# Kernel optimization log

Measured on AMD Instinct MI355X. Metric: run time of the kernel, lower is better.

The kernel has to match this reference:

```python
import jax, jax.numpy as jnp
import numpy as np

B, T, D, N = 16, 1024, 1024, 8


def setup_inputs() -> dict:
    key = jax.random.key(0)
    k1, k2, k3, k4 = jax.random.split(key, 4)
    s = 1.0 / np.sqrt(D)
    return {
        "x": jax.random.normal(k1, (B, T, D), dtype=jnp.float32),
        "W_h": jax.random.normal(k2, (D, D), dtype=jnp.float32) * (0.9 * s),
        "W_x": jax.random.normal(k3, (D, D), dtype=jnp.float32) * s,
        "b_h": jnp.zeros((D,), dtype=jnp.float32),
        "W_write": jax.random.normal(k4, (D, D), dtype=jnp.float32) * s,
    }


def reference(x, W_h, W_x, b_h, W_write):
    Bs, Ts, Ds = x.shape
    scale = 1.0 / Ds ** 0.5
    x_proj = jnp.einsum('btd,ed->bte', x, W_x)  # x @ W_x.T
    h_tape0 = jnp.zeros((Bs, N, Ds), dtype=x.dtype)
    h_work0 = jnp.zeros((Bs, Ds), dtype=x.dtype)

    def step(carry, x_t):
        h_tape, h_work = carry
        read_scores = jnp.einsum('bd,bnd->bn', h_work, h_tape) * scale
        read_attn = jax.nn.softmax(read_scores, axis=-1)
        read_val = jnp.einsum('bn,bnd->bd', read_attn, h_tape)
        Rh = h_work @ W_h.T
        h_work_new = jnp.tanh(x_t + Rh + read_val + b_h)
        write_val = h_work_new @ W_write.T
        write_scores = jnp.einsum('bd,bnd->bn', write_val, h_tape) * scale
        write_attn = jax.nn.softmax(write_scores, axis=-1)
        wa = write_attn[..., None]  # [B,N,1]
        h_tape_new = h_tape * (1.0 - wa) + write_val[:, None, :] * wa
        return (h_tape_new, h_work_new), h_work_new

    (h_tape_final, _), h_work_all = jax.lax.scan(
        step, (h_tape0, h_work0), jnp.swapaxes(x_proj, 0, 1))
    h_work_all = jnp.swapaxes(h_work_all, 0, 1)  # [B,T,D]
    return h_work_all, h_tape_final, h_work_all[:, -1, :]
```

## Files before the change

kernel.cpp:

```cpp
#include <hip/hip_runtime.h>
#include <math.h>

typedef __bf16 bf16x8 __attribute__((ext_vector_type(8)));
typedef float f32x4 __attribute__((ext_vector_type(4)));

namespace {

constexpr int kB = 16;
constexpr int kT = 1024;
constexpr int kD = 1024;
constexpr int kN = 8;
constexpr float kScale = 0.03125f;

constexpr unsigned long long kSent = ~0ull;
constexpr unsigned kSentW = 0xFFFFFFFFu;
constexpr int kHS = 3 * kB * kD;
constexpr int kRW = 2 * kB * kD;

__device__ inline unsigned short f2bf(float f) {
  unsigned u = __float_as_uint(f);
  u += 0x7FFFu + ((u >> 16) & 1u);
  return (unsigned short)(u >> 16);
}
__device__ inline float bf2f(unsigned short b) {
  return __uint_as_float(((unsigned)b) << 16);
}

__device__ inline void atst8(void* p, unsigned long long v) {
  __hip_atomic_store((unsigned long long*)p, v, __ATOMIC_RELAXED,
                     __HIP_MEMORY_SCOPE_AGENT);
}
__device__ inline unsigned long long atld8(const void* p) {
  return __hip_atomic_load((unsigned long long*)p, __ATOMIC_RELAXED,
                           __HIP_MEMORY_SCOPE_AGENT);
}
__device__ inline void atstf(float* p, float v) {
  __hip_atomic_store(p, v, __ATOMIC_RELAXED, __HIP_MEMORY_SCOPE_AGENT);
}
__device__ inline void atstu(unsigned* p, unsigned v) {
  __hip_atomic_store(p, v, __ATOMIC_RELAXED, __HIP_MEMORY_SCOPE_AGENT);
}
__device__ inline unsigned atldu(const unsigned* p) {
  return __hip_atomic_load((unsigned*)p, __ATOMIC_RELAXED,
                           __HIP_MEMORY_SCOPE_AGENT);
}

union U16 { unsigned long long ll[2]; unsigned wrd[4]; bf16x8 bv; float4 f4; };

__global__ __launch_bounds__(256)
void xproj_kernel(const float* __restrict__ X, const float* __restrict__ Wx,
                  float* __restrict__ C) {
  __shared__ float Xs[16][132];
  __shared__ float Ws[16][132];
  const int tid = threadIdx.x;
  const int n0 = blockIdx.x * 128;
  const int m0 = blockIdx.y * 128;
  const int tx = tid & 15;
  const int ty = tid >> 4;
  const int lr = tid >> 2;
  const int lc = (tid & 3) * 4;

  float acc[8][8];
#pragma unroll
  for (int i = 0; i < 8; ++i)
#pragma unroll
    for (int j = 0; j < 8; ++j) acc[i][j] = 0.f;

  for (int k0 = 0; k0 < kD; k0 += 16) {
    const float4 xa = *(const float4*)&X[(size_t)(m0 + lr) * kD + k0 + lc];
    const float4 xb = *(const float4*)&X[(size_t)(m0 + lr + 64) * kD + k0 + lc];
    const float4 wa = *(const float4*)&Wx[(size_t)(n0 + lr) * kD + k0 + lc];
    const float4 wb = *(const float4*)&Wx[(size_t)(n0 + lr + 64) * kD + k0 + lc];
    __syncthreads();
    Xs[lc + 0][lr] = xa.x; Xs[lc + 1][lr] = xa.y; Xs[lc + 2][lr] = xa.z; Xs[lc + 3][lr] = xa.w;
    Xs[lc + 0][lr + 64] = xb.x; Xs[lc + 1][lr + 64] = xb.y; Xs[lc + 2][lr + 64] = xb.z; Xs[lc + 3][lr + 64] = xb.w;
    Ws[lc + 0][lr] = wa.x; Ws[lc + 1][lr] = wa.y; Ws[lc + 2][lr] = wa.z; Ws[lc + 3][lr] = wa.w;
    Ws[lc + 0][lr + 64] = wb.x; Ws[lc + 1][lr + 64] = wb.y; Ws[lc + 2][lr + 64] = wb.z; Ws[lc + 3][lr + 64] = wb.w;
    __syncthreads();
#pragma unroll
    for (int k = 0; k < 16; ++k) {
      float a[8], b[8];
      *(float4*)&a[0] = *(const float4*)&Xs[k][ty * 8];
      *(float4*)&a[4] = *(const float4*)&Xs[k][ty * 8 + 4];
      *(float4*)&b[0] = *(const float4*)&Ws[k][tx * 8];
      *(float4*)&b[4] = *(const float4*)&Ws[k][tx * 8 + 4];
#pragma unroll
      for (int i = 0; i < 8; ++i)
#pragma unroll
        for (int j = 0; j < 8; ++j) acc[i][j] += a[i] * b[j];
    }
  }
#pragma unroll
  for (int i = 0; i < 8; ++i) {
    float4 v0 = make_float4(acc[i][0], acc[i][1], acc[i][2], acc[i][3]);
    float4 v1 = make_float4(acc[i][4], acc[i][5], acc[i][6], acc[i][7]);
    float* p = &C[(size_t)(m0 + ty * 8 + i) * kD + n0 + tx * 8];
    *(float4*)p = v0;
    *(float4*)(p + 4) = v1;
  }
}

__device__ inline void store_split(unsigned short* hs, int b, int d4, float4 h) {
  union { unsigned short u[4]; unsigned long long ll; } c2, c1, c0;
  float hv[4] = {h.x, h.y, h.z, h.w};
#pragma unroll
  for (int e = 0; e < 4; ++e) {
    unsigned short x = f2bf(hv[e]);
    float r = hv[e] - bf2f(x);
    unsigned short y = f2bf(r);
    float r2 = r - bf2f(y);
    unsigned short z = f2bf(r2);
    c2.u[e] = x; c1.u[e] = y; c0.u[e] = z;
  }
  const int w = d4 >> 8;
  const int j = (d4 >> 5) & 7;
  const int q = (d4 >> 3) & 3;
  const int hf = (d4 >> 2) & 1;
  const int off = ((w * 8 + j) << 9) + (hf << 8) + ((q * 16 + b) << 2);
  atst8(&hs[0 * 16384 + off], c2.ll);
  atst8(&hs[1 * 16384 + off], c1.ll);
  atst8(&hs[2 * 16384 + off], c0.ll);
}

__global__ __launch_bounds__(256, 1)
void scan_kernel(const float* __restrict__ Wh, const float* __restrict__ Ww,
                 const float* __restrict__ bh,
                 float* __restrict__ hall,
                 unsigned short* __restrict__ hsplit,
                 float* __restrict__ rw,
                 unsigned* __restrict__ hmark,
                 float* __restrict__ out_tape,
                 float* __restrict__ out_h) {
  const int g = blockIdx.x;
  const int tid = threadIdx.x;
  const int w = tid >> 6;
  const int ln = tid & 63;
  const int bat = ln & 15;
  const int q = ln >> 4;
  const bool tapeb = (g < kB);
  const int col0 = (g & 31) * 32;
  const int matw = g >> 5;

  __shared__ float tp[kN][kD];
  __shared__ f32x4 Cred[2][4][2][64];
  __shared__ float red2[4][16];

  bf16x8 wf[3][2][8];
  {
    const float* Wsrc = matw ? Ww : Wh;
#pragma unroll
    for (int ct = 0; ct < 2; ++ct)
#pragma unroll
      for (int j = 0; j < 8; ++j) {
        const float* src = &Wsrc[(size_t)(col0 + ct * 16 + bat) * kD + (w * 8 + j) * 32 + q * 8];
        float v[8];
        *(float4*)&v[0] = *(const float4*)src;
        *(float4*)&v[4] = *(const float4*)(src + 4);
        union { unsigned short u[8]; bf16x8 b; } e2, e1, e0;
#pragma unroll
        for (int e = 0; e < 8; ++e) {
          unsigned short a = f2bf(v[e]);
          float r = v[e] - bf2f(a);
          unsigned short b2 = f2bf(r);
          float r2 = r - bf2f(b2);
          unsigned short c = f2bf(r2);
          e2.u[e] = a; e1.u[e] = b2; e0.u[e] = c;
        }
        wf[0][ct][j] = e2.b;
        wf[1][ct][j] = e1.b;
        wf[2][ct][j] = e0.b;
      }
  }

  float4 hprev = make_float4(0.f, 0.f, 0.f, 0.f);
  float4 bh4 = make_float4(0.f, 0.f, 0.f, 0.f);
  const int d4 = tid * 4;
  if (tapeb) {
    const size_t x0 = (size_t)g * kT * kD + d4;
    float4 xp0 = *(const float4*)&hall[x0];
    hprev.x = tanhf(xp0.x); hprev.y = tanhf(xp0.y);
    hprev.z = tanhf(xp0.z); hprev.w = tanhf(xp0.w);
    *(float4*)&hall[x0] = hprev;
    store_split(hsplit, g, d4, hprev);
    asm volatile("s_waitcnt vmcnt(0)" ::: "memory");
    if (ln == 0) atstu(&hmark[(w * 16 + g) * 16], 1u);
    bh4 = *(const float4*)&bh[d4];
    float4 z = make_float4(0.f, 0.f, 0.f, 0.f);
#pragma unroll
    for (int i = 0; i < 8; ++i) ((float4*)&tp[0][0])[i * 256 + tid] = z;
    __syncthreads();
  }

  for (int t = 0; t < kT; ++t) {
    const int p = t & 1;
    const unsigned short* hb = hsplit + p * kHS;

    float4 xp4 = make_float4(0.f, 0.f, 0.f, 0.f);
    if (tapeb && t < kT - 1)
      xp4 = *(const float4*)&hall[((size_t)g * kT + (t + 1)) * kD + d4];

    {
      const unsigned need = (unsigned)(t + 1);
      const unsigned* mk = &hmark[(w * 16 + bat) * 16];
      for (;;) {
        unsigned v = 0;
        if (q == 0) v = atldu(mk);
        v = __shfl(v, bat);
        if (v >= need) break;
        __builtin_amdgcn_s_sleep(1);
      }
      asm volatile("" ::: "memory");
    }
    bf16x8 af[3][8];
    const unsigned short* hw0 = hb + (w << 12) + (ln << 2);
#pragma unroll
    for (int j = 0; j < 8; ++j) {
      const unsigned short* p0 = hw0 + (j << 9);
#pragma unroll
      for (int part = 0; part < 3; ++part) {
        U16 u;
        u.ll[0] = atld8(p0 + part * 16384);
        u.ll[1] = atld8(p0 + part * 16384 + 256);
        af[part][j] = u.bv;
      }
    }

    f32x4 zf = {0.f, 0.f, 0.f, 0.f};
    f32x4 acc[2][2] = {{zf, zf}, {zf, zf}};
#pragma unroll
    for (int j = 0; j < 8; ++j) {
      const int s = j & 1;
#pragma unroll
      for (int ct = 0; ct < 2; ++ct) {
        f32x4 a = acc[ct][s];
        a = __builtin_amdgcn_mfma_f32_16x16x32_bf16(af[0][j], wf[0][ct][j], a, 0, 0, 0);
        a = __builtin_amdgcn_mfma_f32_16x16x32_bf16(af[0][j], wf[1][ct][j], a, 0, 0, 0);
        a = __builtin_amdgcn_mfma_f32_16x16x32_bf16(af[1][j], wf[0][ct][j], a, 0, 0, 0);
        a = __builtin_amdgcn_mfma_f32_16x16x32_bf16(af[0][j], wf[2][ct][j], a, 0, 0, 0);
        a = __builtin_amdgcn_mfma_f32_16x16x32_bf16(af[2][j], wf[0][ct][j], a, 0, 0, 0);
        a = __builtin_amdgcn_mfma_f32_16x16x32_bf16(af[1][j], wf[1][ct][j], a, 0, 0, 0);
        acc[ct][s] = a;
      }
    }
    Cred[p][w][0][ln] = acc[0][0] + acc[0][1];
    Cred[p][w][1][ln] = acc[1][0] + acc[1][1];
    __syncthreads();
    if (tid < 128) {
      const int ct = tid >> 6, l2 = tid & 63;
      f32x4 sv = Cred[p][0][ct][l2] + Cred[p][1][ct][l2] +
                 Cred[p][2][ct][l2] + Cred[p][3][ct][l2];
      float* dst = rw + p * kRW + matw * (kB * kD);
      const int col = col0 + ct * 16 + (l2 & 15);
      const int m0 = (l2 >> 4) * 4;
#pragma unroll
      for (int r = 0; r < 4; ++r) atstf(&dst[(size_t)(m0 + r) * kD + col], sv[r]);
    }

    if (!tapeb) continue;

    const int b = g;
    float* rwp = rw + p * kRW;
    float* pr = &rwp[b * kD + d4];
    float* pw = &rwp[kB * kD + b * kD + d4];
    float4 rh4, wv4;
    for (;;) {
      U16 ur, uw;
      ur.ll[0] = atld8(pr); ur.ll[1] = atld8(pr + 2);
      uw.ll[0] = atld8(pw); uw.ll[1] = atld8(pw + 2);
      int bad = 0;
#pragma unroll
      for (int k2 = 0; k2 < 4; ++k2)
        bad |= (ur.wrd[k2] == kSentW) | (uw.wrd[k2] == kSentW);
      if (!bad) { rh4 = ur.f4; wv4 = uw.f4; break; }
      __builtin_amdgcn_s_sleep(1);
    }
    asm volatile("" ::: "memory");
    atst8(pr, kSent); atst8(pr + 2, kSent);
    atst8(pw, kSent); atst8(pw + 2, kSent);

    float part[kN];
#pragma unroll
    for (int n = 0; n < kN; ++n) {
      const float4 tv = *(const float4*)&tp[n][d4];
      part[n] = wv4.x * tv.x + wv4.y * tv.y + wv4.z * tv.z + wv4.w * tv.w;
    }
#pragma unroll
    for (int off = 32; off > 0; off >>= 1)
#pragma unroll
      for (int n = 0; n < kN; ++n) part[n] += __shfl_xor(part[n], off);
    if (ln == 0)
#pragma unroll
      for (int n = 0; n < kN; ++n) red2[w][n] = part[n];
    __syncthreads();

    float wa[kN];
    {
      float mx = -1e30f;
#pragma unroll
      for (int n = 0; n < kN; ++n) {
        const float sc = kScale * (red2[0][n] + red2[1][n] + red2[2][n] + red2[3][n]);
        wa[n] = sc;
        mx = fmaxf(mx, sc);
      }
      float ssum = 0.f;
#pragma unroll
      for (int n = 0; n < kN; ++n) { wa[n] = expf(wa[n] - mx); ssum += wa[n]; }
      const float inv = 1.f / ssum;
#pragma unroll
      for (int n = 0; n < kN; ++n) wa[n] *= inv;
    }

#pragma unroll
    for (int n = 0; n < kN; ++n) {
      float4 tv = *(const float4*)&tp[n][d4];
      const float wn = wa[n], om = 1.f - wn;
      tv.x = tv.x * om + wv4.x * wn; tv.y = tv.y * om + wv4.y * wn;
      tv.z = tv.z * om + wv4.z * wn; tv.w = tv.w * om + wv4.w * wn;
      *(float4*)&tp[n][d4] = tv;
    }

    if (t == kT - 1) {
#pragma unroll
      for (int n = 0; n < kN; ++n) {
        const float4 tv = *(const float4*)&tp[n][d4];
        *(float4*)&out_tape[((size_t)b * kN + n) * kD + d4] = tv;
      }
      *(float4*)&out_h[b * kD + d4] = hprev;
      continue;
    }

#pragma unroll
    for (int n = 0; n < kN; ++n) {
      const float4 tv = *(const float4*)&tp[n][d4];
      part[n] = hprev.x * tv.x + hprev.y * tv.y + hprev.z * tv.z + hprev.w * tv.w;
    }
#pragma unroll
    for (int off = 32; off > 0; off >>= 1)
#pragma unroll
      for (int n = 0; n < kN; ++n) part[n] += __shfl_xor(part[n], off);
    if (ln == 0)
#pragma unroll
      for (int n = 0; n < kN; ++n) red2[w][8 + n] = part[n];
    __syncthreads();

    float ra[kN];
    {
      float mx = -1e30f;
#pragma unroll
      for (int n = 0; n < kN; ++n) {
        const float sc = kScale * (red2[0][8 + n] + red2[1][8 + n] + red2[2][8 + n] + red2[3][8 + n]);
        ra[n] = sc;
        mx = fmaxf(mx, sc);
      }
      float ssum = 0.f;
#pragma unroll
      for (int n = 0; n < kN; ++n) { ra[n] = expf(ra[n] - mx); ssum += ra[n]; }
      const float inv = 1.f / ssum;
#pragma unroll
      for (int n = 0; n < kN; ++n) ra[n] *= inv;
    }

    float4 rv = make_float4(0.f, 0.f, 0.f, 0.f);
#pragma unroll
    for (int n = 0; n < kN; ++n) {
      const float4 tv = *(const float4*)&tp[n][d4];
      rv.x += ra[n] * tv.x; rv.y += ra[n] * tv.y;
      rv.z += ra[n] * tv.z; rv.w += ra[n] * tv.w;
    }

    float4 hn;
    hn.x = tanhf(xp4.x + rh4.x + rv.x + bh4.x);
    hn.y = tanhf(xp4.y + rh4.y + rv.y + bh4.y);
    hn.z = tanhf(xp4.z + rh4.z + rv.z + bh4.z);
    hn.w = tanhf(xp4.w + rh4.w + rv.w + bh4.w);

    *(float4*)&hall[((size_t)b * kT + (t + 1)) * kD + d4] = hn;
    store_split(hsplit + (p ^ 1) * kHS, b, d4, hn);
    hprev = hn;

    asm volatile("s_waitcnt vmcnt(0)" ::: "memory");
    if (ln == 0) atstu(&hmark[(w * 16 + b) * 16], (unsigned)(t + 2));
  }
}

}

extern "C" void kernel_launch(void* const* d_in, const int* in_sizes, int n_in,
                              void* d_out, int out_size, void* d_ws, size_t ws_size,
                              hipStream_t stream) {
  const float* x  = (const float*)d_in[0];
  const float* Wh = (const float*)d_in[1];
  const float* Wx = (const float*)d_in[2];
  const float* bh = (const float*)d_in[3];
  const float* Ww = (const float*)d_in[4];

  float* out = (float*)d_out;
  float* hall = out;
  float* out_tape = out + (size_t)kB * kT * kD;
  float* out_h = out_tape + (size_t)kB * kN * kD;

  unsigned* hmark = (unsigned*)d_ws;
  unsigned short* hsplit = (unsigned short*)((char*)d_ws + 4096);
  float* rw = (float*)((char*)d_ws + 4096 + 2 * kHS * (int)sizeof(unsigned short));

  hipMemsetAsync(d_ws, 0, 4096, stream);
  hipMemsetAsync((void*)rw, 0xFF, 2 * kRW * sizeof(float), stream);

  xproj_kernel<<<dim3(kD / 128, (kB * kT) / 128), 256, 0, stream>>>(x, Wx, hall);

  scan_kernel<<<64, 256, 0, stream>>>(Wh, Ww, bh, hall, hsplit, rw, hmark,
                                      out_tape, out_h);
}
```

Baseline: 10.80 ms.

## Publish per-wave partial sums directly and fold read scores algebraically

Each wave now writes its own MFMA partial tile straight to global memory, so the cross-wave shared-memory reduction and its block barrier on the critical path go away. Consumers sum the four partials themselves. The read-attention scores are derived algebraically from pre-update tape dot products plus an h·write_val term, which merges the two reductions into one barrier. The Rh partials are polled later so the write path overlaps with them. The cost is four times more sentinel polling and global loads per consumer, and a small change in floating-point summation order.

```diff
diff --git a/kernel.cpp b/kernel.cpp
--- a/kernel.cpp
+++ b/kernel.cpp
@@ -15,7 +15,7 @@
 constexpr unsigned long long kSent = ~0ull;
 constexpr unsigned kSentW = 0xFFFFFFFFu;
 constexpr int kHS = 3 * kB * kD;
-constexpr int kRW = 2 * kB * kD;
+constexpr int kRWP = 2 * 32 * 4 * 512;
 
 __device__ inline unsigned short f2bf(float f) {
   unsigned u = __float_as_uint(f);
@@ -142,8 +142,7 @@
   const int matw = g >> 5;
 
   __shared__ float tp[kN][kD];
-  __shared__ f32x4 Cred[2][4][2][64];
-  __shared__ float red2[4][16];
+  __shared__ float red2[2][4][20];
 
   bf16x8 wf[3][2][8];
   {
@@ -171,6 +170,8 @@
         wf[2][ct][j] = e0.b;
       }
   }
+
+  float* const pbase0 = rw + ((size_t)((matw * 32 + (g & 31)) * 4 + w)) * 512;
 
   float4 hprev = make_float4(0.f, 0.f, 0.f, 0.f);
   float4 bh4 = make_float4(0.f, 0.f, 0.f, 0.f);
@@ -194,6 +195,7 @@
   for (int t = 0; t < kT; ++t) {
     const int p = t & 1;
     const unsigned short* hb = hsplit + p * kHS;
+    float* const rwP = rw + (size_t)p * kRWP;
 
     float4 xp4 = make_float4(0.f, 0.f, 0.f, 0.f);
     if (tapeb && t < kT - 1)
@@ -242,113 +244,151 @@
         acc[ct][s] = a;
       }
     }
-    Cred[p][w][0][ln] = acc[0][0] + acc[0][1];
-    Cred[p][w][1][ln] = acc[1][0] + acc[1][1];
+    {
+      const f32x4 a0 = acc[0][0] + acc[0][1];
+      const f32x4 a1 = acc[1][0] + acc[1][1];
+      float* base = pbase0 + (size_t)p * kRWP;
+      const int cc = ln & 15;
+      const int m0r = (ln >> 4) * 4;
+#pragma unroll
+      for (int r = 0; r < 4; ++r) {
+        atstf(&base[(m0r + r) * 32 + cc], a0[r]);
+        atstf(&base[(m0r + r) * 32 + 16 + cc], a1[r]);
+      }
+    }
+
+    if (!tapeb) continue;
+
+    const int b = g;
+    const int cb = d4 >> 5;
+    const int c0 = d4 & 31;
+    float* bwv = rwP + ((size_t)(32 + cb) * 4) * 512 + b * 32 + c0;
+    float* brh = rwP + ((size_t)cb * 4) * 512 + b * 32 + c0;
+
+    U16 vw[4];
+#pragma unroll
+    for (int k = 0; k < 4; ++k) {
+      vw[k].ll[0] = atld8(bwv + k * 512);
+      vw[k].ll[1] = atld8(bwv + k * 512 + 2);
+    }
+
+    {
+      float part[kN];
+#pragma unroll
+      for (int n = 0; n < kN; ++n) {
+        const float4 tv = *(const float4*)&tp[n][d4];
+        part[n] = hprev.x * tv.x + hprev.y * tv.y + hprev.z * tv.z + hprev.w * tv.w;
+      }
+#pragma unroll
+      for (int off = 32; off > 0; off >>= 1)
+#pragma unroll
+        for (int n = 0; n < kN; ++n) part[n] += __shfl_xor(part[n], off);
+      if (ln == 0)
+#pragma unroll
+        for (int n = 0; n < kN; ++n) red2[p][w][8 + n] = part[n];
+    }
+
+    for (;;) {
+      int bad = 0;
+#pragma unroll
+      for (int k = 0; k < 4; ++k)
+#pragma unroll
+        for (int k2 = 0; k2 < 4; ++k2) bad |= (vw[k].wrd[k2] == kSentW);
+      if (!bad) break;
+      __builtin_amdgcn_s_sleep(1);
+#pragma unroll
+      for (int k = 0; k < 4; ++k) {
+        vw[k].ll[0] = atld8(bwv + k * 512);
+        vw[k].ll[1] = atld8(bwv + k * 512 + 2);
+      }
+    }
+    asm volatile("" ::: "memory");
+#pragma unroll
+    for (int k = 0; k < 4; ++k) {
+      atst8(bwv + k * 512, kSent); atst8(bwv + k * 512 + 2, kSent);
+    }
+    float4 wv4;
+    wv4.x = ((vw[0].f4.x + vw[1].f4.x) + vw[2].f4.x) + vw[3].f4.x;
+    wv4.y = ((vw[0].f4.y + vw[1].f4.y) + vw[2].f4.y) + vw[3].f4.y;
+    wv4.z = ((vw[0].f4.z + vw[1].f4.z) + vw[2].f4.z) + vw[3].f4.z;
+    wv4.w = ((vw[0].f4.w + vw[1].f4.w) + vw[2].f4.w) + vw[3].f4.w;
+
+    U16 vr[4];
+#pragma unroll
+    for (int k = 0; k < 4; ++k) {
+      vr[k].ll[0] = atld8(brh + k * 512);
+      vr[k].ll[1] = atld8(brh + k * 512 + 2);
+    }
+
+    {
+      float part[9];
+#pragma unroll
+      for (int n = 0; n < kN; ++n) {
+        const float4 tv = *(const float4*)&tp[n][d4];
+        part[n] = wv4.x * tv.x + wv4.y * tv.y + wv4.z * tv.z + wv4.w * tv.w;
+      }
+      part[8] = hprev.x * wv4.x + hprev.y * wv4.y + hprev.z * wv4.z + hprev.w * wv4.w;
+#pragma unroll
+      for (int off = 32; off > 0; off >>= 1)
+#pragma unroll
+        for (int n = 0; n < 9; ++n) part[n] += __shfl_xor(part[n], off);
+      if (ln == 0) {
+#pragma unroll
+        for (int n = 0; n < kN; ++n) red2[p][w][n] = part[n];
+        red2[p][w][16] = part[8];
+      }
+    }
     __syncthreads();
-    if (tid < 128) {
-      const int ct = tid >> 6, l2 = tid & 63;
-      f32x4 sv = Cred[p][0][ct][l2] + Cred[p][1][ct][l2] +
-                 Cred[p][2][ct][l2] + Cred[p][3][ct][l2];
-      float* dst = rw + p * kRW + matw * (kB * kD);
-      const int col = col0 + ct * 16 + (l2 & 15);
-      const int m0 = (l2 >> 4) * 4;
-#pragma unroll
-      for (int r = 0; r < 4; ++r) atstf(&dst[(size_t)(m0 + r) * kD + col], sv[r]);
-    }
-
-    if (!tapeb) continue;
-
-    const int b = g;
-    float* rwp = rw + p * kRW;
-    float* pr = &rwp[b * kD + d4];
-    float* pw = &rwp[kB * kD + b * kD + d4];
-    float4 rh4, wv4;
-    for (;;) {
-      U16 ur, uw;
-      ur.ll[0] = atld8(pr); ur.ll[1] = atld8(pr + 2);
-      uw.ll[0] = atld8(pw); uw.ll[1] = atld8(pw + 2);
-      int bad = 0;
-#pragma unroll
-      for (int k2 = 0; k2 < 4; ++k2)
-        bad |= (ur.wrd[k2] == kSentW) | (uw.wrd[k2] == kSentW);
-      if (!bad) { rh4 = ur.f4; wv4 = uw.f4; break; }
-      __builtin_amdgcn_s_sleep(1);
-    }
-    asm volatile("" ::: "memory");
-    atst8(pr, kSent); atst8(pr + 2, kSent);
-    atst8(pw, kSent); atst8(pw + 2, kSent);
-
-    float part[kN];
+
+    float s_wv[kN], s_h[kN], s_hwv;
+#pragma unroll
+    for (int n = 0; n < kN; ++n) {
+      s_wv[n] = ((red2[p][0][n] + red2[p][1][n]) + red2[p][2][n]) + red2[p][3][n];
+      s_h[n] = ((red2[p][0][8 + n] + red2[p][1][8 + n]) + red2[p][2][8 + n]) + red2[p][3][8 + n];
+    }
+    s_hwv = ((red2[p][0][16] + red2[p][1][16]) + red2[p][2][16]) + red2[p][3][16];
+
+    float wa[kN];
+    {
+      float mx = -1e30f;
+#pragma unroll
+      for (int n = 0; n < kN; ++n) {
+        const float sc = kScale * s_wv[n];
+        wa[n] = sc;
+        mx = fmaxf(mx, sc);
+      }
+      float ssum = 0.f;
+#pragma unroll
+      for (int n = 0; n < kN; ++n) { wa[n] = expf(wa[n] - mx); ssum += wa[n]; }
+      const float inv = 1.f / ssum;
+#pragma unroll
+      for (int n = 0; n < kN; ++n) wa[n] *= inv;
+    }
+
+    float4 tpn[kN];
 #pragma unroll
     for (int n = 0; n < kN; ++n) {
       const float4 tv = *(const float4*)&tp[n][d4];
-      part[n] = wv4.x * tv.x + wv4.y * tv.y + wv4.z * tv.z + wv4.w * tv.w;
-    }
-#pragma unroll
-    for (int off = 32; off > 0; off >>= 1)
-#pragma unroll
-      for (int n = 0; n < kN; ++n) part[n] += __shfl_xor(part[n], off);
-    if (ln == 0)
-#pragma unroll
-      for (int n = 0; n < kN; ++n) red2[w][n] = part[n];
-    __syncthreads();
-
-    float wa[kN];
-    {
-      float mx = -1e30f;
-#pragma unroll
-      for (int n = 0; n < kN; ++n) {
-        const float sc = kScale * (red2[0][n] + red2[1][n] + red2[2][n] + red2[3][n]);
-        wa[n] = sc;
-        mx = fmaxf(mx, sc);
-      }
-      float ssum = 0.f;
-#pragma unroll
-      for (int n = 0; n < kN; ++n) { wa[n] = expf(wa[n] - mx); ssum += wa[n]; }
-      const float inv = 1.f / ssum;
-#pragma unroll
-      for (int n = 0; n < kN; ++n) wa[n] *= inv;
-    }
-
-#pragma unroll
-    for (int n = 0; n < kN; ++n) {
-      float4 tv = *(const float4*)&tp[n][d4];
       const float wn = wa[n], om = 1.f - wn;
-      tv.x = tv.x * om + wv4.x * wn; tv.y = tv.y * om + wv4.y * wn;
-      tv.z = tv.z * om + wv4.z * wn; tv.w = tv.w * om + wv4.w * wn;
-      *(float4*)&tp[n][d4] = tv;
+      tpn[n].x = tv.x * om + wv4.x * wn; tpn[n].y = tv.y * om + wv4.y * wn;
+      tpn[n].z = tv.z * om + wv4.z * wn; tpn[n].w = tv.w * om + wv4.w * wn;
+      *(float4*)&tp[n][d4] = tpn[n];
     }
 
     if (t == kT - 1) {
 #pragma unroll
-      for (int n = 0; n < kN; ++n) {
-        const float4 tv = *(const float4*)&tp[n][d4];
-        *(float4*)&out_tape[((size_t)b * kN + n) * kD + d4] = tv;
-      }
+      for (int n = 0; n < kN; ++n)
+        *(float4*)&out_tape[((size_t)b * kN + n) * kD + d4] = tpn[n];
       *(float4*)&out_h[b * kD + d4] = hprev;
       continue;
     }
 
-#pragma unroll
-    for (int n = 0; n < kN; ++n) {
-      const float4 tv = *(const float4*)&tp[n][d4];
-      part[n] = hprev.x * tv.x + hprev.y * tv.y + hprev.z * tv.z + hprev.w * tv.w;
-    }
-#pragma unroll
-    for (int off = 32; off > 0; off >>= 1)
-#pragma unroll
-      for (int n = 0; n < kN; ++n) part[n] += __shfl_xor(part[n], off);
-    if (ln == 0)
-#pragma unroll
-      for (int n = 0; n < kN; ++n) red2[w][8 + n] = part[n];
-    __syncthreads();
-
     float ra[kN];
     {
       float mx = -1e30f;
 #pragma unroll
       for (int n = 0; n < kN; ++n) {
-        const float sc = kScale * (red2[0][8 + n] + red2[1][8 + n] + red2[2][8 + n] + red2[3][8 + n]);
+        const float sc = kScale * (s_h[n] * (1.f - wa[n]) + s_hwv * wa[n]);
         ra[n] = sc;
         mx = fmaxf(mx, sc);
       }
@@ -363,10 +403,34 @@
     float4 rv = make_float4(0.f, 0.f, 0.f, 0.f);
 #pragma unroll
     for (int n = 0; n < kN; ++n) {
-      const float4 tv = *(const float4*)&tp[n][d4];
-      rv.x += ra[n] * tv.x; rv.y += ra[n] * tv.y;
-      rv.z += ra[n] * tv.z; rv.w += ra[n] * tv.w;
-    }
+      rv.x += ra[n] * tpn[n].x; rv.y += ra[n] * tpn[n].y;
+      rv.z += ra[n] * tpn[n].z; rv.w += ra[n] * tpn[n].w;
+    }
+
+    for (;;) {
+      int bad = 0;
+#pragma unroll
+      for (int k = 0; k < 4; ++k)
+#pragma unroll
+        for (int k2 = 0; k2 < 4; ++k2) bad |= (vr[k].wrd[k2] == kSentW);
+      if (!bad) break;
+      __builtin_amdgcn_s_sleep(1);
+#pragma unroll
+      for (int k = 0; k < 4; ++k) {
+        vr[k].ll[0] = atld8(brh + k * 512);
+        vr[k].ll[1] = atld8(brh + k * 512 + 2);
+      }
+    }
+    asm volatile("" ::: "memory");
+#pragma unroll
+    for (int k = 0; k < 4; ++k) {
+      atst8(brh + k * 512, kSent); atst8(brh + k * 512 + 2, kSent);
+    }
+    float4 rh4;
+    rh4.x = ((vr[0].f4.x + vr[1].f4.x) + vr[2].f4.x) + vr[3].f4.x;
+    rh4.y = ((vr[0].f4.y + vr[1].f4.y) + vr[2].f4.y) + vr[3].f4.y;
+    rh4.z = ((vr[0].f4.z + vr[1].f4.z) + vr[2].f4.z) + vr[3].f4.z;
+    rh4.w = ((vr[0].f4.w + vr[1].f4.w) + vr[2].f4.w) + vr[3].f4.w;
 
     float4 hn;
     hn.x = tanhf(xp4.x + rh4.x + rv.x + bh4.x);
@@ -404,7 +468,7 @@
   float* rw = (float*)((char*)d_ws + 4096 + 2 * kHS * (int)sizeof(unsigned short));
 
   hipMemsetAsync(d_ws, 0, 4096, stream);
-  hipMemsetAsync((void*)rw, 0xFF, 2 * kRW * sizeof(float), stream);
+  hipMemsetAsync((void*)rw, 0xFF, 2 * kRWP * sizeof(float), stream);
 
   xproj_kernel<<<dim3(kD / 128, (kB * kT) / 128), 256, 0, stream>>>(x, Wx, hall);
 
```

Measured after the change: 10.92 ms. No clear change (+1.2%).

## Use sentinel-poisoned hidden-state buffer to validate reads instead of strict flag ordering

Applied to the files above, without the earlier changes.

The split bf16 hidden-state buffer is now poisoned with a sentinel value, both at launch and after each consumer has read it. Readers spin until none of the loaded words equals the sentinel, so data validity is checked directly rather than relying only on the marker flag. The hall store is moved after the marker update, so the next step's consumers are signalled earlier. This adds extra sentinel stores and retry loads per step, and a valid bf16 pattern could in principle collide with the sentinel.

```diff
diff --git a/kernel.cpp b/kernel.cpp
--- a/kernel.cpp
+++ b/kernel.cpp
@@ -211,19 +211,28 @@
       }
       asm volatile("" ::: "memory");
     }
-    bf16x8 af[3][8];
+    U16 uf[3][8];
     const unsigned short* hw0 = hb + (w << 12) + (ln << 2);
-#pragma unroll
-    for (int j = 0; j < 8; ++j) {
-      const unsigned short* p0 = hw0 + (j << 9);
-#pragma unroll
-      for (int part = 0; part < 3; ++part) {
-        U16 u;
-        u.ll[0] = atld8(p0 + part * 16384);
-        u.ll[1] = atld8(p0 + part * 16384 + 256);
-        af[part][j] = u.bv;
-      }
-    }
+    for (;;) {
+      int bad = 0;
+#pragma unroll
+      for (int j = 0; j < 8; ++j) {
+        const unsigned short* p0 = hw0 + (j << 9);
+#pragma unroll
+        for (int part = 0; part < 3; ++part) {
+          uf[part][j].ll[0] = atld8(p0 + part * 16384);
+          uf[part][j].ll[1] = atld8(p0 + part * 16384 + 256);
+        }
+      }
+#pragma unroll
+      for (int j = 0; j < 8; ++j)
+#pragma unroll
+        for (int part = 0; part < 3; ++part)
+          bad |= (uf[part][j].ll[0] == kSent) | (uf[part][j].ll[1] == kSent);
+      if (!bad) break;
+      __builtin_amdgcn_s_sleep(1);
+    }
+    asm volatile("" ::: "memory");
 
     f32x4 zf = {0.f, 0.f, 0.f, 0.f};
     f32x4 acc[2][2] = {{zf, zf}, {zf, zf}};
@@ -233,12 +242,12 @@
 #pragma unroll
       for (int ct = 0; ct < 2; ++ct) {
         f32x4 a = acc[ct][s];
-        a = __builtin_amdgcn_mfma_f32_16x16x32_bf16(af[0][j], wf[0][ct][j], a, 0, 0, 0);
-        a = __builtin_amdgcn_mfma_f32_16x16x32_bf16(af[0][j], wf[1][ct][j], a, 0, 0, 0);
-        a = __builtin_amdgcn_mfma_f32_16x16x32_bf16(af[1][j], wf[0][ct][j], a, 0, 0, 0);
-        a = __builtin_amdgcn_mfma_f32_16x16x32_bf16(af[0][j], wf[2][ct][j], a, 0, 0, 0);
-        a = __builtin_amdgcn_mfma_f32_16x16x32_bf16(af[2][j], wf[0][ct][j], a, 0, 0, 0);
-        a = __builtin_amdgcn_mfma_f32_16x16x32_bf16(af[1][j], wf[1][ct][j], a, 0, 0, 0);
+        a = __builtin_amdgcn_mfma_f32_16x16x32_bf16(uf[0][j].bv, wf[0][ct][j], a, 0, 0, 0);
+        a = __builtin_amdgcn_mfma_f32_16x16x32_bf16(uf[0][j].bv, wf[1][ct][j], a, 0, 0, 0);
+        a = __builtin_amdgcn_mfma_f32_16x16x32_bf16(uf[1][j].bv, wf[0][ct][j], a, 0, 0, 0);
+        a = __builtin_amdgcn_mfma_f32_16x16x32_bf16(uf[0][j].bv, wf[2][ct][j], a, 0, 0, 0);
+        a = __builtin_amdgcn_mfma_f32_16x16x32_bf16(uf[2][j].bv, wf[0][ct][j], a, 0, 0, 0);
+        a = __builtin_amdgcn_mfma_f32_16x16x32_bf16(uf[1][j].bv, wf[1][ct][j], a, 0, 0, 0);
         acc[ct][s] = a;
       }
     }
@@ -293,6 +302,15 @@
       for (int n = 0; n < kN; ++n) red2[w][n] = part[n];
     __syncthreads();
 
+    {
+      unsigned short* hp0 = hsplit + p * kHS;
+      const int off = (((d4 >> 8) * 8 + ((d4 >> 5) & 7)) << 9) +
+                      (((d4 >> 2) & 1) << 8) + ((((d4 >> 3) & 3) * 16 + b) << 2);
+      atst8(&hp0[0 * 16384 + off], kSent);
+      atst8(&hp0[1 * 16384 + off], kSent);
+      atst8(&hp0[2 * 16384 + off], kSent);
+    }
+
     float wa[kN];
     {
       float mx = -1e30f;
@@ -374,12 +392,11 @@
     hn.z = tanhf(xp4.z + rh4.z + rv.z + bh4.z);
     hn.w = tanhf(xp4.w + rh4.w + rv.w + bh4.w);
 
+    asm volatile("s_waitcnt vmcnt(0)" ::: "memory");
+    store_split(hsplit + (p ^ 1) * kHS, b, d4, hn);
+    if (ln == 0) atstu(&hmark[(w * 16 + b) * 16], (unsigned)(t + 2));
     *(float4*)&hall[((size_t)b * kT + (t + 1)) * kD + d4] = hn;
-    store_split(hsplit + (p ^ 1) * kHS, b, d4, hn);
     hprev = hn;
-
-    asm volatile("s_waitcnt vmcnt(0)" ::: "memory");
-    if (ln == 0) atstu(&hmark[(w * 16 + b) * 16], (unsigned)(t + 2));
   }
 }
 
@@ -404,7 +421,9 @@
   float* rw = (float*)((char*)d_ws + 4096 + 2 * kHS * (int)sizeof(unsigned short));
 
   hipMemsetAsync(d_ws, 0, 4096, stream);
-  hipMemsetAsync((void*)rw, 0xFF, 2 * kRW * sizeof(float), stream);
+  hipMemsetAsync((char*)d_ws + 4096, 0xFF,
+                 2 * kHS * sizeof(unsigned short) + 2 * kRW * sizeof(float),
+                 stream);
 
   xproj_kernel<<<dim3(kD / 128, (kB * kT) / 128), 256, 0, stream>>>(x, Wx, hall);
 
```

Result: faster. 10.08 ms (-6.6%).
